# Optimization experiments

Measured on AMD Instinct MI355X. Metric: run time of the kernel, lower is better.

## Reference

```python
import jax, jax.numpy as jnp
import numpy as np

NEG_SLOPE = 0.1   # LeakyReLU slope
EPS = 1e-5        # GroupNorm eps
GROUPS = 8        # out_feat // 16 = 128 // 16
NSAMPLE = 16      # naggre (k in KNN)
FEAT = 128        # feat_dim


def leaky(x):
    return jnp.where(x >= 0, x, NEG_SLOPE * x)


def gnorm(x, gamma, beta):
    # GroupNorm over channel dim 1; works for [B,C,N] and [B,C,N,K]
    B, C = x.shape[0], x.shape[1]
    sh = x.shape
    xg = x.reshape(B, GROUPS, -1)
    m = xg.mean(-1, keepdims=True)
    v = xg.var(-1, keepdims=True)
    xg = (xg - m) * jax.lax.rsqrt(v + EPS)
    br = (1, C) + (1,) * (len(sh) - 2)
    return xg.reshape(sh) * gamma.reshape(br) + beta.reshape(br)


def conv1(x, W, b):  # 1x1 Conv1d: x [B,C,N]
    return jnp.einsum('oc,bcn->bon', W, x) + b[None, :, None]


def conv2(x, W, b):  # 1x1 Conv2d: x [B,C,N,K]
    return jnp.einsum('oc,bcnk->bonk', W, x) + b[None, :, None, None]


def knn_idx(xyz, k):
    # xyz [B,3,N] -> idx [B,N,k] of k nearest points (self included)
    pts = xyz.transpose(0, 2, 1)                      # [B,N,3]
    sq = jnp.sum(pts * pts, axis=-1)                  # [B,N]
    d2 = sq[:, :, None] + sq[:, None, :] - 2.0 * jnp.einsum('bnc,bmc->bnm', pts, pts)
    _, idx = jax.lax.top_k(-d2, k)
    return idx


# grouping_operation: feat [B,C,N], idx [B,N,K] -> [B,C,N,K]
group = jax.vmap(lambda f, i: f[:, i])


def setup_inputs() -> dict:
    key = jax.random.key(0)
    ks = jax.random.split(key, 32)
    s = 0.05
    d = {
        'xyz': jax.random.normal(ks[0], (2, 3, 8192), jnp.float32),
        'feat': jax.random.normal(ks[1], (2, FEAT, 8192), jnp.float32),
        'W_pre': jax.random.normal(ks[2], (FEAT, FEAT), jnp.float32) * s,
        'b_pre': jnp.zeros((FEAT,), jnp.float32),
        'W_pos1': jax.random.normal(ks[3], (FEAT, 3), jnp.float32) * s,
        'b_pos1': jnp.zeros((FEAT,), jnp.float32),
        'g_pos1': jnp.ones((FEAT,), jnp.float32),
        'be_pos1': jnp.zeros((FEAT,), jnp.float32),
        'W_pos2': jax.random.normal(ks[4], (FEAT, FEAT), jnp.float32) * s,
        'b_pos2': jnp.zeros((FEAT,), jnp.float32),
        'W_q': jax.random.normal(ks[5], (FEAT, FEAT), jnp.float32) * s,
        'b_q': jnp.zeros((FEAT,), jnp.float32),
        'W_k': jax.random.normal(ks[6], (FEAT, FEAT), jnp.float32) * s,
        'b_k': jnp.zeros((FEAT,), jnp.float32),
        'W_v': jax.random.normal(ks[7], (FEAT, FEAT), jnp.float32) * s,
        'b_v': jnp.zeros((FEAT,), jnp.float32),
        'W_att1': jax.random.normal(ks[8], (FEAT, FEAT), jnp.float32) * s,
        'b_att1': jnp.zeros((FEAT,), jnp.float32),
        'g_att1': jnp.ones((FEAT,), jnp.float32),
        'be_att1': jnp.zeros((FEAT,), jnp.float32),
        'W_att2': jax.random.normal(ks[9], (FEAT, FEAT), jnp.float32) * s,
        'b_att2': jnp.zeros((FEAT,), jnp.float32),
        'W_post': jax.random.normal(ks[10], (FEAT, FEAT), jnp.float32) * s,
        'b_post': jnp.zeros((FEAT,), jnp.float32),
        'g_post': jnp.ones((FEAT,), jnp.float32),
        'be_post': jnp.zeros((FEAT,), jnp.float32),
    }
    return d


def reference(xyz, feat, W_pre, b_pre, W_pos1, b_pos1, g_pos1, be_pos1,
              W_pos2, b_pos2, W_q, b_q, W_k, b_k, W_v, b_v,
              W_att1, b_att1, g_att1, be_att1, W_att2, b_att2,
              W_post, b_post, g_post, be_post):
    idx = knn_idx(xyz, NSAMPLE)                       # [B,N,K]
    new_feat = conv1(feat, W_pre, b_pre)              # [B,C,N]
    rel = group(xyz, idx) - xyz[:, :, :, None]        # [B,3,N,K]
    pos = conv2(rel, W_pos1, b_pos1)
    pos = leaky(gnorm(pos, g_pos1, be_pos1))
    pos = conv2(pos, W_pos2, b_pos2)                  # [B,C,N,K]
    q = conv1(new_feat, W_q, b_q)
    k = group(conv1(new_feat, W_k, b_k), idx)
    v = group(conv1(new_feat, W_v, b_v), idx)
    att = q[:, :, :, None] - k + pos
    att = conv2(att, W_att1, b_att1)
    att = leaky(gnorm(att, g_att1, be_att1))
    att = conv2(att, W_att2, b_att2)
    att = jax.nn.softmax(att, axis=3)                 # softmax over neighbors
    out = jnp.sum(att * v, axis=3) + new_feat         # [B,C,N]
    out = leaky(gnorm(conv1(out, W_post, b_post), g_post, be_post))
    return out
```

## Files before the change

### kernel.cpp

```cpp
#include <hip/hip_runtime.h>
#include <hip/hip_bf16.h>
#include <float.h>

#define B_ 2
#define N_ 8192
#define C_ 128
#define K_ 16
#define G_ 8
#define NK_ (N_*K_)
#define BN_ (B_*N_)
#define BNK_ (B_*NK_)
#define CN_ (C_*N_)
#define NEG 0.1f
#define EPSV 1e-5f

typedef __attribute__((ext_vector_type(4))) float f32x4;
typedef __attribute__((ext_vector_type(8))) short s16x8;
typedef __attribute__((ext_vector_type(4))) short s16x4;

__device__ __forceinline__ float leakyf(float x){ return x >= 0.f ? x : NEG*x; }
__device__ __forceinline__ short f2b(float x){
  union { __hip_bfloat16 b; short s; } u; u.b = __float2bfloat16(x); return u.s;
}
__device__ __forceinline__ float b2f(short s){
  union { __hip_bfloat16 b; short s; } u; u.s = s; return __bfloat162float(u.b);
}

__device__ __forceinline__ int dpp_shr1_i(int x){
  return __builtin_amdgcn_update_dpp(x, x, 0x111, 0xF, 0xF, false);
}
__device__ __forceinline__ double dpp_shr1_d(double x){
  union { double d; int i[2]; } u; u.d = x;
  u.i[0] = dpp_shr1_i(u.i[0]);
  u.i[1] = dpp_shr1_i(u.i[1]);
  return u.d;
}
__device__ __forceinline__ double readlane_d(double x, int l){
  union { double d; int i[2]; } u; u.d = x;
  union { double d; int i[2]; } r;
  r.i[0] = __builtin_amdgcn_readlane(u.i[0], l);
  r.i[1] = __builtin_amdgcn_readlane(u.i[1], l);
  return r.d;
}

__global__ __launch_bounds__(256) void pack_kernel(const float* __restrict__ xyz, float4* __restrict__ pt4){
  int e = blockIdx.x*256 + threadIdx.x;
  int b = e >> 13, n = e & (N_-1);
  const float* xb = xyz + b*3*N_;
  float x = xb[n], y = xb[N_+n], z = xb[2*N_+n];
  pt4[e] = make_float4(x, y, z, x*x + y*y + z*z);
}

#define KNN_TPB 512
#define KNN_CHUNK 2048
#define KNN_MARGIN 5e-4f
__global__ __launch_bounds__(KNN_TPB) void knn_kernel(const float4* __restrict__ pt4, int* __restrict__ idxo){
  __shared__ float4 sp[KNN_CHUNK];
  int lane = threadIdx.x & 63, wid = threadIdx.x >> 6;
  int qg = blockIdx.x*(KNN_TPB/64) + wid;
  int b = qg >> 13, n = qg & (N_-1);
  const float4* pts = pt4 + b*N_;
  float4 qp = pts[n];
  double qx = qp.x, qy = qp.y, qz = qp.z;
  double qsq = qx*qx + qy*qy + qz*qz;
  float qx2 = -2.f*qp.x, qy2 = -2.f*qp.y, qz2 = -2.f*qp.z;
  double myd = DBL_MAX; int myi = 0x7fffffff;
  float cmpv = FLT_MAX;

  auto process = [&](unsigned long long m, double d2v, int base){
    while (m){
      int src = __ffsll(m) - 1; m &= m - 1;
      double dn = readlane_d(d2v, src);
      int in_ = base + src;
      bool less = (dn < myd) || (dn == myd && in_ < myi);
      unsigned long long bm = __ballot(less) & 0xFFFFull;
      if (bm){
        int pos = __ffsll(bm) - 1;
        double pd = dpp_shr1_d(myd);
        int pi = dpp_shr1_i(myi);
        if (lane < 16){
          if (lane > pos){ myd = pd; myi = pi; }
          else if (lane == pos){ myd = dn; myi = in_; }
        }
      }
    }
  };

  for (int c0 = 0; c0 < N_; c0 += KNN_CHUNK){
    __syncthreads();
    #pragma unroll
    for (int t = 0; t < KNN_CHUNK/KNN_TPB; t++){
      int i = t*KNN_TPB + threadIdx.x;
      sp[i] = pts[c0 + i];
    }
    __syncthreads();
    for (int j0 = 0; j0 < KNN_CHUNK; j0 += 128){
      float4 pA = sp[j0 + lane];
      float4 pB = sp[j0 + 64 + lane];
      float fA = fmaf(pA.x, qx2, fmaf(pA.y, qy2, fmaf(pA.z, qz2, pA.w)));
      float fB = fmaf(pB.x, qx2, fmaf(pB.y, qy2, fmaf(pB.z, qz2, pB.w)));
      unsigned long long mA = __ballot(fA < cmpv);
      unsigned long long mB = __ballot(fB < cmpv);
      if (mA | mB){
        if (mA){
          double px = pA.x, py = pA.y, pz = pA.z;
          double psq = px*px + py*py + pz*pz;
          double dot = qx*px + qy*py + qz*pz;
          double d2 = qsq + psq - 2.0*dot;
          process(mA, d2, c0 + j0);
        }
        if (mB){
          double px = pB.x, py = pB.y, pz = pB.z;
          double psq = px*px + py*py + pz*pz;
          double dot = qx*px + qy*py + qz*pz;
          double d2 = qsq + psq - 2.0*dot;
          process(mB, d2, c0 + j0 + 64);
        }
        double thr = readlane_d(myd, 15);
        cmpv = (float)(thr - qsq) + KNN_MARGIN;
      }
    }
  }
  if (lane < 16) idxo[qg*K_ + lane] = myi;
}

__global__ __launch_bounds__(256) void featb_kernel(const float* __restrict__ feat, ushort* __restrict__ fb){
  int p = blockIdx.x*256 + threadIdx.x;
  int b = p >> 13, n = p & (N_-1);
  const float* xin = feat + b*CN_ + n;
  #pragma unroll
  for (int c0 = 0; c0 < C_; c0 += 8){
    s16x8 o8;
    #pragma unroll
    for (int i = 0; i < 8; i++) o8[i] = f2b(xin[(size_t)(c0+i)*N_]);
    *(s16x8*)(fb + (size_t)p*C_ + c0) = o8;
  }
}

__global__ __launch_bounds__(256) void setup_kernel(const float* __restrict__ W_att1,
    const float* __restrict__ W_pos2, const float* __restrict__ W_q, const float* __restrict__ W_k,
    const float* __restrict__ b_pos2, const float* __restrict__ b_att1,
    const float* __restrict__ b_q, const float* __restrict__ b_k,
    float* __restrict__ Wf, float* __restrict__ Wqa, float* __restrict__ Wka,
    float* __restrict__ bG1, float* __restrict__ bqa, float* __restrict__ bka){
  int bx = blockIdx.x;
  if (bx < 192){
    int which = bx >> 6;
    const float* Bm = which==0 ? W_pos2 : (which==1 ? W_q : W_k);
    float* Cm = which==0 ? Wf : (which==1 ? Wqa : Wka);
    int e = (bx & 63)*256 + threadIdx.x;
    int o = e >> 7, c = e & 127;
    float s = 0.f;
    #pragma unroll 8
    for (int m = 0; m < 128; m++) s += W_att1[o*128+m]*Bm[m*128+c];
    Cm[e] = s;
  } else {
    for (int t = threadIdx.x; t < 384; t += 256){
      int which = t >> 7, o = t & 127;
      const float* v = which==0 ? b_pos2 : (which==1 ? b_q : b_k);
      float* out = which==0 ? bG1 : (which==1 ? bqa : bka);
      float s = which==0 ? b_att1[o] : 0.f;
      for (int m = 0; m < 128; m++) s += W_att1[o*128+m]*v[m];
      out[o] = s;
    }
  }
}

__global__ __launch_bounds__(256) void pos_stats_kernel(const float4* __restrict__ pt4,
    const int* __restrict__ idx, const float* __restrict__ W1, const float* __restrict__ b1,
    float* __restrict__ gsum, float* __restrict__ gssq){
  __shared__ float ls[G_], lss[G_];
  if (threadIdx.x < G_){ ls[threadIdx.x] = 0.f; lss[threadIdx.x] = 0.f; }
  __syncthreads();
  int p = blockIdx.x*256 + threadIdx.x;
  int b = p >> 17;
  int n = p >> 4;
  int j = idx[p];
  float4 pj = pt4[(b<<13) + j], pn = pt4[n];
  float rx = pj.x - pn.x, ry = pj.y - pn.y, rz = pj.z - pn.z;
  #pragma unroll
  for (int g = 0; g < G_; g++){
    float s = 0.f, ss = 0.f;
    #pragma unroll
    for (int ci = 0; ci < 16; ci++){
      int c = g*16 + ci;
      float v = b1[c] + W1[3*c]*rx + W1[3*c+1]*ry + W1[3*c+2]*rz;
      s += v; ss += v*v;
    }
    #pragma unroll
    for (int mk = 32; mk; mk >>= 1){ s += __shfl_xor(s, mk, 64); ss += __shfl_xor(ss, mk, 64); }
    if ((threadIdx.x & 63) == 0){ atomicAdd(&ls[g], s); atomicAdd(&lss[g], ss); }
  }
  __syncthreads();
  if (threadIdx.x < G_){
    atomicAdd(&gsum[b*G_ + threadIdx.x], ls[threadIdx.x]);
    atomicAdd(&gssq[b*G_ + threadIdx.x], lss[threadIdx.x]);
  }
}

__global__ void posfin_kernel(const float* __restrict__ gsum, const float* __restrict__ gssq,
    const float* __restrict__ W1, const float* __restrict__ b1,
    const float* __restrict__ g1, const float* __restrict__ be1, float* __restrict__ prm, float invcnt){
  __shared__ float sm[16], sr[16];
  int i = threadIdx.x;
  if (i < 16){
    float m = gsum[i]*invcnt;
    float v = gssq[i]*invcnt - m*m;
    v = fmaxf(v, 0.f);
    sm[i] = m; sr[i] = rsqrtf(v + EPSV);
  }
  __syncthreads();
  int b = i >> 7, c = i & 127, g = c >> 4;
  float rs = sr[b*G_+g]*g1[c];
  prm[b*512 +   0 + c] = W1[3*c]*rs;
  prm[b*512 + 128 + c] = W1[3*c+1]*rs;
  prm[b*512 + 256 + c] = W1[3*c+2]*rs;
  prm[b*512 + 384 + c] = (b1[c]-sm[b*G_+g])*rs + be1[c];
}

__global__ void attfin_kernel(const float* __restrict__ gsum, const float* __restrict__ gssq,
    const float* __restrict__ ga, const float* __restrict__ bea, float* __restrict__ prm, float invcnt){
  __shared__ float sm[16], sr[16];
  int i = threadIdx.x;
  if (i < 16){
    float m = gsum[i]*invcnt;
    float v = gssq[i]*invcnt - m*m;
    v = fmaxf(v, 0.f);
    sm[i] = m; sr[i] = rsqrtf(v + EPSV);
  }
  __syncthreads();
  int b = i >> 7, c = i & 127, g = c >> 4;
  float sc = ga[c]*sr[b*G_+g];
  prm[b*256 +   0 + c] = sc;
  prm[b*256 + 128 + c] = bea[c] - sm[b*G_+g]*sc;
}

#define ST_COPY 0
#define ST_GN   1
#define ST_POS  2
#define EP_PM    0
#define EP_QKS   1
#define EP_F32CM 2

template<int STAGE, int EPI>
__device__ __forceinline__ void mgemm_body(ushort* xs, float* sblk,
    const ushort* __restrict__ Xb, const float* __restrict__ W, const float* __restrict__ bias,
    const float* __restrict__ prm, const float4* __restrict__ pt4, const int* __restrict__ idx,
    const ushort* __restrict__ Aq, const ushort* __restrict__ Ak,
    void* __restrict__ Y, float* __restrict__ gsum, float* __restrict__ gssq, int bsh, int bx)
{
  int tid = threadIdx.x;
  int l = tid & 63, wid = tid >> 6;
  int lm = l & 15, lh = l >> 4;
  int p0 = bx * 64;
  int b = p0 >> bsh;

  if (tid < 16) sblk[tid] = 0.f;

  s16x8 afr[2][4];
  #pragma unroll
  for (int t = 0; t < 2; t++){
    int T = wid*2 + t;
    #pragma unroll
    for (int ks = 0; ks < 4; ks++){
      const float* wr = W + (size_t)(T*16 + lm)*C_ + ks*32 + lh*8;
      float4 w0 = *(const float4*)wr;
      float4 w1 = *(const float4*)(wr+4);
      s16x8 a;
      a[0]=f2b(w0.x); a[1]=f2b(w0.y); a[2]=f2b(w0.z); a[3]=f2b(w0.w);
      a[4]=f2b(w1.x); a[5]=f2b(w1.y); a[6]=f2b(w1.z); a[7]=f2b(w1.w);
      afr[t][ks] = a;
    }
  }

  {
    int row = tid & 63, cc = tid >> 6;
    if constexpr (STAGE == ST_COPY){
      const ushort* src = Xb + (size_t)(p0+row)*C_ + cc*32;
      #pragma unroll
      for (int q = 0; q < 4; q++){
        s16x8 v8 = *(const s16x8*)(src + q*8);
        int sl = (cc*4+q) ^ (row&7);
        *(s16x8*)(xs + row*C_ + sl*8) = v8;
      }
    } else if constexpr (STAGE == ST_GN){
      const ushort* src = Xb + (size_t)(p0+row)*C_ + cc*32;
      const float* sc = prm + b*256;
      const float* sh = prm + b*256 + 128;
      #pragma unroll
      for (int q = 0; q < 4; q++){
        s16x8 v8 = *(const s16x8*)(src + q*8);
        s16x8 o8;
        #pragma unroll
        for (int i = 0; i < 8; i++){
          int c = cc*32 + q*8 + i;
          o8[i] = f2b(leakyf(b2f(v8[i])*sc[c] + sh[c]));
        }
        int sl = (cc*4+q) ^ (row&7);
        *(s16x8*)(xs + row*C_ + sl*8) = o8;
      }
    } else {
      int p = p0 + row;
      int ng = p >> 4;
      int j = idx[p];
      float4 pj = pt4[(b<<13) + j], pn = pt4[ng];
      float rx = pj.x - pn.x, ry = pj.y - pn.y, rz = pj.z - pn.z;
      const float* sx = prm + b*512;
      const float* sy = sx + 128;
      const float* sz = sx + 256;
      const float* so = sx + 384;
      #pragma unroll
      for (int q = 0; q < 4; q++){
        s16x8 o8;
        #pragma unroll
        for (int i = 0; i < 8; i++){
          int c = cc*32 + q*8 + i;
          o8[i] = f2b(leakyf(sx[c]*rx + sy[c]*ry + sz[c]*rz + so[c]));
        }
        int sl = (cc*4+q) ^ (row&7);
        *(s16x8*)(xs + row*C_ + sl*8) = o8;
      }
    }
  }
  __syncthreads();

  f32x4 acc[2][4];
  #pragma unroll
  for (int t = 0; t < 2; t++){
    f32x4 bs = *(const f32x4*)(bias + (wid*2+t)*16 + lh*4);
    #pragma unroll
    for (int ps = 0; ps < 4; ps++) acc[t][ps] = bs;
  }
  #pragma unroll
  for (int ps = 0; ps < 4; ps++){
    int row = ps*16 + lm;
    s16x8 bf[4];
    #pragma unroll
    for (int ks = 0; ks < 4; ks++){
      int sl = (ks*4+lh) ^ (row&7);
      bf[ks] = *(const s16x8*)(xs + row*C_ + sl*8);
    }
    #pragma unroll
    for (int ks = 0; ks < 4; ks++){
      #pragma unroll
      for (int t = 0; t < 2; t++)
        acc[t][ps] = __builtin_amdgcn_mfma_f32_16x16x32_bf16(afr[t][ks], bf[ks], acc[t][ps], 0,0,0);
    }
  }

  float gs[2] = {0.f,0.f}, gq[2] = {0.f,0.f};
  #pragma unroll
  for (int t = 0; t < 2; t++){
    int T = wid*2 + t;
    int o0 = T*16 + lh*4;
    #pragma unroll
    for (int ps = 0; ps < 4; ps++){
      int p = p0 + ps*16 + lm;
      if constexpr (EPI == EP_PM){
        s16x4 r4;
        #pragma unroll
        for (int r = 0; r < 4; r++) r4[r] = f2b(acc[t][ps][r]);
        *(s16x4*)((ushort*)Y + (size_t)p*C_ + o0) = r4;
      } else if constexpr (EPI == EP_QKS){
        int ng = p >> 4;
        int j = idx[p];
        s16x4 aq4 = *(const s16x4*)(Aq + (size_t)ng*C_ + o0);
        s16x4 ak4 = *(const s16x4*)(Ak + ((size_t)(b<<13)+j)*C_ + o0);
        s16x4 r4;
        #pragma unroll
        for (int r = 0; r < 4; r++){
          float v = acc[t][ps][r] + b2f(aq4[r]) - b2f(ak4[r]);
          r4[r] = f2b(v);
          gs[t] += v; gq[t] += v*v;
        }
        *(s16x4*)((ushort*)Y + (size_t)p*C_ + o0) = r4;
      } else {
        float* yf = (float*)Y;
        #pragma unroll
        for (int r = 0; r < 4; r++){
          float v = acc[t][ps][r];
          yf[(size_t)(o0+r)*BN_ + p] = v;
          gs[t] += v; gq[t] += v*v;
        }
      }
    }
  }

  if constexpr (EPI == EP_QKS || EPI == EP_F32CM){
    #pragma unroll
    for (int t = 0; t < 2; t++){
      float s = gs[t], q = gq[t];
      #pragma unroll
      for (int mk = 32; mk; mk >>= 1){ s += __shfl_xor(s, mk, 64); q += __shfl_xor(q, mk, 64); }
      if (l == 0){
        int T = wid*2 + t;
        atomicAdd(&sblk[T], s); atomicAdd(&sblk[8+T], q);
      }
    }
    __syncthreads();
    if (tid < 8){
      atomicAdd(&gsum[b*G_ + tid], sblk[tid]);
      atomicAdd(&gssq[b*G_ + tid], sblk[8+tid]);
    }
  }
}

template<int STAGE, int EPI>
__global__ __launch_bounds__(256) void mgemm_kernel(
    const ushort* __restrict__ Xb, const float* __restrict__ W, const float* __restrict__ bias,
    const float* __restrict__ prm, const float4* __restrict__ pt4, const int* __restrict__ idx,
    const ushort* __restrict__ Aq, const ushort* __restrict__ Ak,
    void* __restrict__ Y, float* __restrict__ gsum, float* __restrict__ gssq, int bsh)
{
  __shared__ ushort xs[64*128];
  __shared__ float sblk[16];
  mgemm_body<STAGE,EPI>(xs, sblk, Xb, W, bias, prm, pt4, idx, Aq, Ak, Y, gsum, gssq, bsh, blockIdx.x);
}

__global__ __launch_bounds__(256) void qkv_kernel(const ushort* __restrict__ nfb,
    const float* __restrict__ Wv, const float* __restrict__ bv,
    const float* __restrict__ Wqa, const float* __restrict__ bqa,
    const float* __restrict__ Wka, const float* __restrict__ bka,
    ushort* __restrict__ vb, ushort* __restrict__ Aqb, ushort* __restrict__ Akb)
{
  __shared__ ushort xs[64*128];
  __shared__ float sblk[16];
  if (blockIdx.y == 0)
    mgemm_body<ST_COPY,EP_PM>(xs, sblk, nfb, Wv, bv, nullptr, nullptr, nullptr, nullptr, nullptr, vb, nullptr, nullptr, 13, blockIdx.x);
  else if (blockIdx.y == 1)
    mgemm_body<ST_COPY,EP_PM>(xs, sblk, nfb, Wqa, bqa, nullptr, nullptr, nullptr, nullptr, nullptr, Aqb, nullptr, nullptr, 13, blockIdx.x);
  else
    mgemm_body<ST_COPY,EP_PM>(xs, sblk, nfb, Wka, bka, nullptr, nullptr, nullptr, nullptr, nullptr, Akb, nullptr, nullptr, 13, blockIdx.x);
}

__global__ __launch_bounds__(256) void att2b_kernel(const ushort* __restrict__ a2s,
    const ushort* __restrict__ vb, const ushort* __restrict__ nfb,
    const int* __restrict__ idx, ushort* __restrict__ outb){
  int tid = blockIdx.x*256 + threadIdx.x;
  int n = tid >> 4;
  int cc = tid & 15;
  int b = n >> 13;
  const int* ir = idx + (size_t)n*16;
  float sum[8], pv[8];
  #pragma unroll
  for (int i = 0; i < 8; i++){ sum[i] = 0.f; pv[i] = 0.f; }
  const ushort* ab = a2s + (size_t)n*16*C_ + cc*8;
  #pragma unroll
  for (int k = 0; k < 16; k++){
    s16x8 l8 = *(const s16x8*)(ab + k*C_);
    int j = ir[k];
    s16x8 v8 = *(const s16x8*)(vb + ((size_t)(b<<13)+j)*C_ + cc*8);
    #pragma unroll
    for (int i = 0; i < 8; i++){
      float e = __expf(b2f(l8[i]));
      sum[i] += e;
      pv[i] += e*b2f(v8[i]);
    }
  }
  s16x8 n8 = *(const s16x8*)(nfb + (size_t)n*C_ + cc*8);
  s16x8 o8;
  #pragma unroll
  for (int i = 0; i < 8; i++) o8[i] = f2b(pv[i]/sum[i] + b2f(n8[i]));
  *(s16x8*)(outb + (size_t)n*C_ + cc*8) = o8;
}

__global__ __launch_bounds__(256) void final_kernel(const float* __restrict__ out1,
    const float* __restrict__ gsum, const float* __restrict__ gssq,
    const float* __restrict__ g, const float* __restrict__ be, float* __restrict__ out){
  int e = blockIdx.x*256 + threadIdx.x;
  int b = e >> 20;
  int c = (e >> 13) & (C_-1);
  int n = e & (N_-1);
  int gi = b*G_ + (c >> 4);
  const float invcnt = 1.0f/(float)(16*N_);
  float m = gsum[gi]*invcnt;
  float var = gssq[gi]*invcnt - m*m;
  var = fmaxf(var, 0.f);
  float r = rsqrtf(var + EPSV);
  float v = (out1[(size_t)c*BN_ + b*N_ + n] - m) * r;
  v = v*g[c] + be[c];
  out[e] = leakyf(v);
}

extern "C" void kernel_launch(void* const* d_in, const int* in_sizes, int n_in,
                              void* d_out, int out_size, void* d_ws, size_t ws_size,
                              hipStream_t stream) {
  const float* xyz    = (const float*)d_in[0];
  const float* feat   = (const float*)d_in[1];
  const float* W_pre  = (const float*)d_in[2];
  const float* b_pre  = (const float*)d_in[3];
  const float* W_pos1 = (const float*)d_in[4];
  const float* b_pos1 = (const float*)d_in[5];
  const float* g_pos1 = (const float*)d_in[6];
  const float* be_pos1= (const float*)d_in[7];
  const float* W_pos2 = (const float*)d_in[8];
  const float* b_pos2 = (const float*)d_in[9];
  const float* W_q    = (const float*)d_in[10];
  const float* b_q    = (const float*)d_in[11];
  const float* W_k    = (const float*)d_in[12];
  const float* b_k    = (const float*)d_in[13];
  const float* W_v    = (const float*)d_in[14];
  const float* b_v    = (const float*)d_in[15];
  const float* W_att1 = (const float*)d_in[16];
  const float* b_att1 = (const float*)d_in[17];
  const float* g_att1 = (const float*)d_in[18];
  const float* be_att1= (const float*)d_in[19];
  const float* W_att2 = (const float*)d_in[20];
  const float* b_att2 = (const float*)d_in[21];
  const float* W_post = (const float*)d_in[22];
  const float* b_post = (const float*)d_in[23];
  const float* g_post = (const float*)d_in[24];
  const float* be_post= (const float*)d_in[25];

  char* w = (char*)d_ws;
  float4* pt4 = (float4*)w;            w += sizeof(float4)*BN_;
  int* idx = (int*)w;                  w += sizeof(int)*BNK_;
  ushort* fb   = (ushort*)w;           w += (size_t)2*BN_*C_;
  ushort* nfb  = (ushort*)w;           w += (size_t)2*BN_*C_;
  ushort* vb   = (ushort*)w;           w += (size_t)2*BN_*C_;
  ushort* Aqb  = (ushort*)w;           w += (size_t)2*BN_*C_;
  ushort* Akb  = (ushort*)w;           w += (size_t)2*BN_*C_;
  ushort* outb = (ushort*)w;           w += (size_t)2*BN_*C_;
  float* out1  = (float*)w;            w += (size_t)4*BN_*C_;
  ushort* bufA = (ushort*)w;           w += (size_t)2*BNK_*C_;
  ushort* bufB = (ushort*)w;           w += (size_t)2*BNK_*C_;
  float* Wf    = (float*)w;            w += sizeof(float)*C_*C_;
  float* Wqa   = (float*)w;            w += sizeof(float)*C_*C_;
  float* Wka   = (float*)w;            w += sizeof(float)*C_*C_;
  float* bG1   = (float*)w;            w += 512;
  float* bqa   = (float*)w;            w += 512;
  float* bka   = (float*)w;            w += 512;
  float* posPrm= (float*)w;            w += sizeof(float)*1024;
  float* attPrm= (float*)w;            w += sizeof(float)*512;
  float* stats = (float*)w;            w += 1024;

  float* pos_sum = stats +  0, *pos_ssq = stats + 16;
  float* att_sum = stats + 64, *att_ssq = stats + 80;
  float* post_sum= stats +128, *post_ssq= stats +144;

  hipMemsetAsync(stats, 0, 1024, stream);

  pack_kernel<<<BN_/256, 256, 0, stream>>>(xyz, pt4);
  knn_kernel<<<BN_/(KNN_TPB/64), KNN_TPB, 0, stream>>>(pt4, idx);
  featb_kernel<<<BN_/256, 256, 0, stream>>>(feat, fb);

  setup_kernel<<<193, 256, 0, stream>>>(W_att1, W_pos2, W_q, W_k, b_pos2, b_att1, b_q, b_k,
      Wf, Wqa, Wka, bG1, bqa, bka);

  mgemm_kernel<ST_COPY,EP_PM><<<BN_/64, 256, 0, stream>>>(fb, W_pre, b_pre, nullptr, nullptr, nullptr,
      nullptr, nullptr, nfb, nullptr, nullptr, 13);
  qkv_kernel<<<dim3(BN_/64, 3), 256, 0, stream>>>(nfb, W_v, b_v, Wqa, bqa, Wka, bka, vb, Aqb, Akb);

  pos_stats_kernel<<<BNK_/256, 256, 0, stream>>>(pt4, idx, W_pos1, b_pos1, pos_sum, pos_ssq);
  posfin_kernel<<<1, 256, 0, stream>>>(pos_sum, pos_ssq, W_pos1, b_pos1, g_pos1, be_pos1, posPrm,
      1.0f/(float)(16.0*NK_));

  mgemm_kernel<ST_POS,EP_QKS><<<BNK_/64, 256, 0, stream>>>(nullptr, Wf, bG1, posPrm, pt4, idx,
      Aqb, Akb, bufA, att_sum, att_ssq, 17);
  attfin_kernel<<<1, 256, 0, stream>>>(att_sum, att_ssq, g_att1, be_att1, attPrm, 1.0f/(float)(16.0*NK_));

  mgemm_kernel<ST_GN,EP_PM><<<BNK_/64, 256, 0, stream>>>(bufA, W_att2, b_att2, attPrm, nullptr, nullptr,
      nullptr, nullptr, bufB, nullptr, nullptr, 17);

  att2b_kernel<<<BN_*16/256, 256, 0, stream>>>(bufB, vb, nfb, idx, outb);

  mgemm_kernel<ST_COPY,EP_F32CM><<<BN_/64, 256, 0, stream>>>(outb, W_post, b_post, nullptr, nullptr, nullptr,
      nullptr, nullptr, out1, post_sum, post_ssq, 13);
  final_kernel<<<(B_*CN_)/256, 256, 0, stream>>>(out1, post_sum, post_ssq, g_post, be_post, (float*)d_out);
}
```

Measured before the change: 413.1 us.

## Fuse att2 GEMM with softmax-weighted aggregation and seed KNN threshold

Replaces the separate att2 GEMM (which wrote a bf16 [BNK,C] buffer) plus the softmax/aggregate kernel with one kernel. It applies exp to the MFMA accumulators, reduces over the 16 neighbours with lane shuffles, and writes the output directly, removing a large intermediate write and read. The KNN kernel now seeds its top-16 list by bitonic-sorting the first 64 candidates and uses a tighter filter margin, so more candidates are rejected early. Risks include extra shuffle traffic in the fused epilogue and possible selection mismatches from the smaller margin. Softmax is computed without max subtraction, as before.

New measurement: 368.4 us. 1.12x faster.

```diff
diff --git a/kernel.cpp b/kernel.cpp
--- a/kernel.cpp
+++ b/kernel.cpp
@@ -53,7 +53,7 @@
 
 #define KNN_TPB 512
 #define KNN_CHUNK 2048
-#define KNN_MARGIN 5e-4f
+#define KNN_MARGIN 2e-4f
 __global__ __launch_bounds__(KNN_TPB) void knn_kernel(const float4* __restrict__ pt4, int* __restrict__ idxo){
   __shared__ float4 sp[KNN_CHUNK];
   int lane = threadIdx.x & 63, wid = threadIdx.x >> 6;
@@ -64,8 +64,33 @@
   double qx = qp.x, qy = qp.y, qz = qp.z;
   double qsq = qx*qx + qy*qy + qz*qz;
   float qx2 = -2.f*qp.x, qy2 = -2.f*qp.y, qz2 = -2.f*qp.z;
-  double myd = DBL_MAX; int myi = 0x7fffffff;
-  float cmpv = FLT_MAX;
+  double myd; int myi;
+  float cmpv;
+
+  {
+    float4 pp = pts[lane];
+    double px = pp.x, py = pp.y, pz = pp.z;
+    double psq = px*px + py*py + pz*pz;
+    double dot = qx*px + qy*py + qz*pz;
+    double d2l = qsq + psq - 2.0*dot;
+    int il = lane;
+    #pragma unroll
+    for (int k2 = 2; k2 <= 64; k2 <<= 1){
+      #pragma unroll
+      for (int mm = k2>>1; mm > 0; mm >>= 1){
+        double pd = __shfl_xor(d2l, mm, 64);
+        int pi = __shfl_xor(il, mm, 64);
+        bool up = ((lane & k2) == 0);
+        bool lower = ((lane & mm) == 0);
+        bool myLess = (d2l < pd) || (d2l == pd && il < pi);
+        bool keep = lower ? (up ? myLess : !myLess) : (up ? !myLess : myLess);
+        if (!keep){ d2l = pd; il = pi; }
+      }
+    }
+    myd = d2l; myi = il;
+    double thr0 = readlane_d(myd, 15);
+    cmpv = (float)(thr0 - qsq) + KNN_MARGIN;
+  }
 
   auto process = [&](unsigned long long m, double d2v, int base){
     while (m){
@@ -101,6 +126,7 @@
       float fB = fmaf(pB.x, qx2, fmaf(pB.y, qy2, fmaf(pB.z, qz2, pB.w)));
       unsigned long long mA = __ballot(fA < cmpv);
       unsigned long long mB = __ballot(fB < cmpv);
+      if (c0 == 0 && j0 == 0) mA = 0;
       if (mA | mB){
         if (mA){
           double px = pA.x, py = pA.y, pz = pA.z;
@@ -242,6 +268,105 @@
 #define EP_QKS   1
 #define EP_F32CM 2
 
+template<int STAGE>
+__device__ __forceinline__ void stage_x(ushort* xs,
+    const ushort* __restrict__ Xb, const float* __restrict__ prm,
+    const float4* __restrict__ pt4, const int* __restrict__ idx, int p0, int b)
+{
+  int tid = threadIdx.x;
+  int row = tid & 63, cc = tid >> 6;
+  if constexpr (STAGE == ST_COPY){
+    const ushort* src = Xb + (size_t)(p0+row)*C_ + cc*32;
+    #pragma unroll
+    for (int q = 0; q < 4; q++){
+      s16x8 v8 = *(const s16x8*)(src + q*8);
+      int sl = (cc*4+q) ^ (row&7);
+      *(s16x8*)(xs + row*C_ + sl*8) = v8;
+    }
+  } else if constexpr (STAGE == ST_GN){
+    const ushort* src = Xb + (size_t)(p0+row)*C_ + cc*32;
+    const float* sc = prm + b*256;
+    const float* sh = prm + b*256 + 128;
+    #pragma unroll
+    for (int q = 0; q < 4; q++){
+      s16x8 v8 = *(const s16x8*)(src + q*8);
+      s16x8 o8;
+      #pragma unroll
+      for (int i = 0; i < 8; i++){
+        int c = cc*32 + q*8 + i;
+        o8[i] = f2b(leakyf(b2f(v8[i])*sc[c] + sh[c]));
+      }
+      int sl = (cc*4+q) ^ (row&7);
+      *(s16x8*)(xs + row*C_ + sl*8) = o8;
+    }
+  } else {
+    int p = p0 + row;
+    int ng = p >> 4;
+    int j = idx[p];
+    float4 pj = pt4[(b<<13) + j], pn = pt4[ng];
+    float rx = pj.x - pn.x, ry = pj.y - pn.y, rz = pj.z - pn.z;
+    const float* sx = prm + b*512;
+    const float* sy = sx + 128;
+    const float* sz = sx + 256;
+    const float* so = sx + 384;
+    #pragma unroll
+    for (int q = 0; q < 4; q++){
+      s16x8 o8;
+      #pragma unroll
+      for (int i = 0; i < 8; i++){
+        int c = cc*32 + q*8 + i;
+        o8[i] = f2b(leakyf(sx[c]*rx + sy[c]*ry + sz[c]*rz + so[c]));
+      }
+      int sl = (cc*4+q) ^ (row&7);
+      *(s16x8*)(xs + row*C_ + sl*8) = o8;
+    }
+  }
+}
+
+__device__ __forceinline__ void load_afr(s16x8 afr[2][4], const float* __restrict__ W, int wid, int lm, int lh){
+  #pragma unroll
+  for (int t = 0; t < 2; t++){
+    int T = wid*2 + t;
+    #pragma unroll
+    for (int ks = 0; ks < 4; ks++){
+      const float* wr = W + (size_t)(T*16 + lm)*C_ + ks*32 + lh*8;
+      float4 w0 = *(const float4*)wr;
+      float4 w1 = *(const float4*)(wr+4);
+      s16x8 a;
+      a[0]=f2b(w0.x); a[1]=f2b(w0.y); a[2]=f2b(w0.z); a[3]=f2b(w0.w);
+      a[4]=f2b(w1.x); a[5]=f2b(w1.y); a[6]=f2b(w1.z); a[7]=f2b(w1.w);
+      afr[t][ks] = a;
+    }
+  }
+}
+
+__device__ __forceinline__ void mfma_tile(f32x4 acc[2][4], const s16x8 afr[2][4],
+    const ushort* xs, const float* __restrict__ bias, int wid, int lm, int lh)
+{
+  #pragma unroll
+  for (int t = 0; t < 2; t++){
+    f32x4 bs = *(const f32x4*)(bias + (wid*2+t)*16 + lh*4);
+    #pragma unroll
+    for (int ps = 0; ps < 4; ps++) acc[t][ps] = bs;
+  }
+  #pragma unroll
+  for (int ps = 0; ps < 4; ps++){
+    int row = ps*16 + lm;
+    s16x8 bf[4];
+    #pragma unroll
+    for (int ks = 0; ks < 4; ks++){
+      int sl = (ks*4+lh) ^ (row&7);
+      bf[ks] = *(const s16x8*)(xs + row*C_ + sl*8);
+    }
+    #pragma unroll
+    for (int ks = 0; ks < 4; ks++){
+      #pragma unroll
+      for (int t = 0; t < 2; t++)
+        acc[t][ps] = __builtin_amdgcn_mfma_f32_16x16x32_bf16(afr[t][ks], bf[ks], acc[t][ps], 0,0,0);
+    }
+  }
+}
+
 template<int STAGE, int EPI>
 __device__ __forceinline__ void mgemm_body(ushort* xs, float* sblk,
     const ushort* __restrict__ Xb, const float* __restrict__ W, const float* __restrict__ bias,
@@ -258,95 +383,12 @@
   if (tid < 16) sblk[tid] = 0.f;
 
   s16x8 afr[2][4];
-  #pragma unroll
-  for (int t = 0; t < 2; t++){
-    int T = wid*2 + t;
-    #pragma unroll
-    for (int ks = 0; ks < 4; ks++){
-      const float* wr = W + (size_t)(T*16 + lm)*C_ + ks*32 + lh*8;
-      float4 w0 = *(const float4*)wr;
-      float4 w1 = *(const float4*)(wr+4);
-      s16x8 a;
-      a[0]=f2b(w0.x); a[1]=f2b(w0.y); a[2]=f2b(w0.z); a[3]=f2b(w0.w);
-      a[4]=f2b(w1.x); a[5]=f2b(w1.y); a[6]=f2b(w1.z); a[7]=f2b(w1.w);
-      afr[t][ks] = a;
-    }
-  }
-
-  {
-    int row = tid & 63, cc = tid >> 6;
-    if constexpr (STAGE == ST_COPY){
-      const ushort* src = Xb + (size_t)(p0+row)*C_ + cc*32;
-      #pragma unroll
-      for (int q = 0; q < 4; q++){
-        s16x8 v8 = *(const s16x8*)(src + q*8);
-        int sl = (cc*4+q) ^ (row&7);
-        *(s16x8*)(xs + row*C_ + sl*8) = v8;
-      }
-    } else if constexpr (STAGE == ST_GN){
-      const ushort* src = Xb + (size_t)(p0+row)*C_ + cc*32;
-      const float* sc = prm + b*256;
-      const float* sh = prm + b*256 + 128;
-      #pragma unroll
-      for (int q = 0; q < 4; q++){
-        s16x8 v8 = *(const s16x8*)(src + q*8);
-        s16x8 o8;
-        #pragma unroll
-        for (int i = 0; i < 8; i++){
-          int c = cc*32 + q*8 + i;
-          o8[i] = f2b(leakyf(b2f(v8[i])*sc[c] + sh[c]));
-        }
-        int sl = (cc*4+q) ^ (row&7);
-        *(s16x8*)(xs + row*C_ + sl*8) = o8;
-      }
-    } else {
-      int p = p0 + row;
-      int ng = p >> 4;
-      int j = idx[p];
-      float4 pj = pt4[(b<<13) + j], pn = pt4[ng];
-      float rx = pj.x - pn.x, ry = pj.y - pn.y, rz = pj.z - pn.z;
-      const float* sx = prm + b*512;
-      const float* sy = sx + 128;
-      const float* sz = sx + 256;
-      const float* so = sx + 384;
-      #pragma unroll
-      for (int q = 0; q < 4; q++){
-        s16x8 o8;
-        #pragma unroll
-        for (int i = 0; i < 8; i++){
-          int c = cc*32 + q*8 + i;
-          o8[i] = f2b(leakyf(sx[c]*rx + sy[c]*ry + sz[c]*rz + so[c]));
-        }
-        int sl = (cc*4+q) ^ (row&7);
-        *(s16x8*)(xs + row*C_ + sl*8) = o8;
-      }
-    }
-  }
+  load_afr(afr, W, wid, lm, lh);
+  stage_x<STAGE>(xs, Xb, prm, pt4, idx, p0, b);
   __syncthreads();
 
   f32x4 acc[2][4];
-  #pragma unroll
-  for (int t = 0; t < 2; t++){
-    f32x4 bs = *(const f32x4*)(bias + (wid*2+t)*16 + lh*4);
-    #pragma unroll
-    for (int ps = 0; ps < 4; ps++) acc[t][ps] = bs;
-  }
-  #pragma unroll
-  for (int ps = 0; ps < 4; ps++){
-    int row = ps*16 + lm;
-    s16x8 bf[4];
-    #pragma unroll
-    for (int ks = 0; ks < 4; ks++){
-      int sl = (ks*4+lh) ^ (row&7);
-      bf[ks] = *(const s16x8*)(xs + row*C_ + sl*8);
-    }
-    #pragma unroll
-    for (int ks = 0; ks < 4; ks++){
-      #pragma unroll
-      for (int t = 0; t < 2; t++)
-        acc[t][ps] = __builtin_amdgcn_mfma_f32_16x16x32_bf16(afr[t][ks], bf[ks], acc[t][ps], 0,0,0);
-    }
-  }
+  mfma_tile(acc, afr, xs, bias, wid, lm, lh);
 
   float gs[2] = {0.f,0.f}, gq[2] = {0.f,0.f};
   #pragma unroll
@@ -433,35 +475,59 @@
     mgemm_body<ST_COPY,EP_PM>(xs, sblk, nfb, Wka, bka, nullptr, nullptr, nullptr, nullptr, nullptr, Akb, nullptr, nullptr, 13, blockIdx.x);
 }
 
-__global__ __launch_bounds__(256) void att2b_kernel(const ushort* __restrict__ a2s,
-    const ushort* __restrict__ vb, const ushort* __restrict__ nfb,
-    const int* __restrict__ idx, ushort* __restrict__ outb){
-  int tid = blockIdx.x*256 + threadIdx.x;
-  int n = tid >> 4;
-  int cc = tid & 15;
-  int b = n >> 13;
-  const int* ir = idx + (size_t)n*16;
-  float sum[8], pv[8];
+__global__ __launch_bounds__(256) void fatt_kernel(const ushort* __restrict__ Xb ,
+    const float* __restrict__ W , const float* __restrict__ bias ,
+    const float* __restrict__ prm , const int* __restrict__ idx,
+    const ushort* __restrict__ vb, const ushort* __restrict__ nfb, ushort* __restrict__ outb)
+{
+  __shared__ ushort xs[64*128];
+  int tid = threadIdx.x;
+  int l = tid & 63, wid = tid >> 6;
+  int lm = l & 15, lh = l >> 4;
+  int p0 = blockIdx.x * 64;
+  int b = p0 >> 17;
+
+  s16x8 afr[2][4];
+  load_afr(afr, W, wid, lm, lh);
+  stage_x<ST_GN>(xs, Xb, prm, nullptr, nullptr, p0, b);
+  __syncthreads();
+
+  f32x4 acc[2][4];
+  mfma_tile(acc, afr, xs, bias, wid, lm, lh);
+
   #pragma unroll
-  for (int i = 0; i < 8; i++){ sum[i] = 0.f; pv[i] = 0.f; }
-  const ushort* ab = a2s + (size_t)n*16*C_ + cc*8;
-  #pragma unroll
-  for (int k = 0; k < 16; k++){
-    s16x8 l8 = *(const s16x8*)(ab + k*C_);
-    int j = ir[k];
-    s16x8 v8 = *(const s16x8*)(vb + ((size_t)(b<<13)+j)*C_ + cc*8);
-    #pragma unroll
-    for (int i = 0; i < 8; i++){
-      float e = __expf(b2f(l8[i]));
-      sum[i] += e;
-      pv[i] += e*b2f(v8[i]);
-    }
-  }
-  s16x8 n8 = *(const s16x8*)(nfb + (size_t)n*C_ + cc*8);
-  s16x8 o8;
-  #pragma unroll
-  for (int i = 0; i < 8; i++) o8[i] = f2b(pv[i]/sum[i] + b2f(n8[i]));
-  *(s16x8*)(outb + (size_t)n*C_ + cc*8) = o8;
+  for (int t = 0; t < 2; t++){
+    int o0 = (wid*2+t)*16 + lh*4;
+    #pragma unroll
+    for (int ps = 0; ps < 4; ps++){
+      int p = p0 + ps*16 + lm;
+      int j = idx[p];
+      s16x4 v4 = *(const s16x4*)(vb + ((size_t)(b<<13)+j)*C_ + o0);
+      f32x4 e, pv;
+      #pragma unroll
+      for (int r = 0; r < 4; r++){
+        float ev = __expf(acc[t][ps][r]);
+        e[r] = ev;
+        pv[r] = ev * b2f(v4[r]);
+      }
+      #pragma unroll
+      for (int mk = 1; mk < 16; mk <<= 1){
+        #pragma unroll
+        for (int r = 0; r < 4; r++){
+          e[r]  += __shfl_xor(e[r], mk, 64);
+          pv[r] += __shfl_xor(pv[r], mk, 64);
+        }
+      }
+      if (lm == 0){
+        int n = p >> 4;
+        s16x4 n4 = *(const s16x4*)(nfb + (size_t)n*C_ + o0);
+        s16x4 o4;
+        #pragma unroll
+        for (int r = 0; r < 4; r++) o4[r] = f2b(pv[r]/e[r] + b2f(n4[r]));
+        *(s16x4*)(outb + (size_t)n*C_ + o0) = o4;
+      }
+    }
+  }
 }
 
 __global__ __launch_bounds__(256) void final_kernel(const float* __restrict__ out1,
@@ -523,7 +589,6 @@
   ushort* outb = (ushort*)w;           w += (size_t)2*BN_*C_;
   float* out1  = (float*)w;            w += (size_t)4*BN_*C_;
   ushort* bufA = (ushort*)w;           w += (size_t)2*BNK_*C_;
-  ushort* bufB = (ushort*)w;           w += (size_t)2*BNK_*C_;
   float* Wf    = (float*)w;            w += sizeof(float)*C_*C_;
   float* Wqa   = (float*)w;            w += sizeof(float)*C_*C_;
   float* Wka   = (float*)w;            w += sizeof(float)*C_*C_;
@@ -559,10 +624,7 @@
       Aqb, Akb, bufA, att_sum, att_ssq, 17);
   attfin_kernel<<<1, 256, 0, stream>>>(att_sum, att_ssq, g_att1, be_att1, attPrm, 1.0f/(float)(16.0*NK_));
 
-  mgemm_kernel<ST_GN,EP_PM><<<BNK_/64, 256, 0, stream>>>(bufA, W_att2, b_att2, attPrm, nullptr, nullptr,
-      nullptr, nullptr, bufB, nullptr, nullptr, 17);
-
-  att2b_kernel<<<BN_*16/256, 256, 0, stream>>>(bufB, vb, nfb, idx, outb);
+  fatt_kernel<<<BNK_/64, 256, 0, stream>>>(bufA, W_att2, b_att2, attPrm, idx, vb, nfb, outb);
 
   mgemm_kernel<ST_COPY,EP_F32CM><<<BN_/64, 256, 0, stream>>>(outb, W_post, b_post, nullptr, nullptr, nullptr,
       nullptr, nullptr, out1, post_sum, post_ssq, 13);
```
